# Optimization experiments

Hardware: AMD Instinct MI355X
Metric: run time of the kernel (lower is better)

## Reference

```python
import jax, jax.numpy as jnp
import numpy as np

THRE = 0.0
VOXEL = (160.0, 160.0)
MAX_N = 100  # module caps N at 100


def setup_inputs() -> dict:
    key = jax.random.key(0)
    k1, k2, k3 = jax.random.split(key, 3)
    # boxes in meters, scaled so BEV coords (x + W/2)/voxel fall inside [-1,1]
    pred_box_infra = jax.random.normal(k1, (100, 8, 3), dtype=jnp.float32) * 20.0
    pred_score_infra = jax.random.uniform(k2, (100,), dtype=jnp.float32)
    infra_features = jax.random.normal(k3, (1, 256, 256, 256), dtype=jnp.float32)
    return {
        "pred_box_infra": pred_box_infra,
        "pred_score_infra": pred_score_infra,
        "infra_features": infra_features,
    }


def _grid_sample_points(feat, grid):
    """torch.F.grid_sample (bilinear, zero padding, align_corners=False)
    specialized to a point list. feat: [C,H,W], grid: [N,2] with (x,y) in [-1,1].
    Returns [C,N]."""
    C, H, W = feat.shape
    ix = ((grid[:, 0] + 1.0) * W - 1.0) / 2.0
    iy = ((grid[:, 1] + 1.0) * H - 1.0) / 2.0
    x0 = jnp.floor(ix)
    y0 = jnp.floor(iy)
    x1 = x0 + 1.0
    y1 = y0 + 1.0
    wx1 = ix - x0
    wx0 = 1.0 - wx1
    wy1 = iy - y0
    wy0 = 1.0 - wy1

    def gather(xf, yf):
        xi = xf.astype(jnp.int32)
        yi = yf.astype(jnp.int32)
        valid = (xi >= 0) & (xi < W) & (yi >= 0) & (yi < H)
        xi = jnp.clip(xi, 0, W - 1)
        yi = jnp.clip(yi, 0, H - 1)
        v = feat[:, yi, xi]  # [C,N]
        return v * valid.astype(feat.dtype)

    return (gather(x0, y0) * (wx0 * wy0)
            + gather(x1, y0) * (wx1 * wy0)
            + gather(x0, y1) * (wx0 * wy1)
            + gather(x1, y1) * (wx1 * wy1))


def reference(pred_box_infra, pred_score_infra, infra_features):
    B, C, H, W = infra_features.shape
    # threshold filter; size=MAX_N keeps shapes static (all boxes pass by construction)
    idx = jnp.nonzero(pred_score_infra > THRE, size=MAX_N, fill_value=0)[0]
    boxes = pred_box_infra[idx]              # [N,8,3]
    N = MAX_N

    l = boxes.min(axis=1)                    # [N,3]
    r = boxes.max(axis=1)                    # [N,3]
    center = (l + r) / 2.0

    lx = (l[:, 0] + W / 2.0) / VOXEL[0]
    ly = (l[:, 1] + H / 2.0) / VOXEL[1]
    rx = (r[:, 0] + W / 2.0) / VOXEL[0]
    ry = (r[:, 1] + H / 2.0) / VOXEL[1]
    bev_size = (ry - ly) * (rx - lx)         # [N]

    cx = (center[:, 0] + W / 2.0) / VOXEL[0]
    cy = (center[:, 1] + H / 2.0) / VOXEL[1]
    grid = jnp.stack([cx, cy], axis=1)       # [N,2]

    cpf = _grid_sample_points(infra_features[0], grid)  # [C,N]

    X = jnp.arange(W, dtype=jnp.float32)
    Y = jnp.arange(H, dtype=jnp.float32)
    # gaussian exponent maps (no exp in original): [N,H,W]
    g = ((X[None, None, :] - cx[:, None, None]) ** 2
         + (Y[None, :, None] - cy[:, None, None]) ** 2) / (2.0 * bev_size[:, None, None] ** 2)

    out = jnp.einsum('cn,nhw->chw', cpf, g) / N  # [C,H,W]
    return out[None]                              # [1,C,H,W]
```

## Files before the change

### kernel.cpp

```cpp
#include <hip/hip_runtime.h>

namespace {

constexpr int CH    = 256;
constexpr int HH    = 256;
constexpr int WW    = 256;
constexpr int NBOX  = 100;
constexpr int MAXN  = 100;
constexpr int BLOCK = 512;
constexpr int SPLIT = 2;

__global__ __launch_bounds__(BLOCK) void comm_kernel(
    const float* __restrict__ boxes,
    const float* __restrict__ scores,
    const float* __restrict__ feat,
    float* __restrict__ out)
{
    __shared__ float sh_a[NBOX], sh_cx[NBOX], sh_cy[NBOX];
    __shared__ float sh_w00[NBOX], sh_w10[NBOX], sh_w01[NBOX], sh_w11[NBOX];
    __shared__ int   sh_t00[NBOX], sh_t10[NBOX], sh_t01[NBOX], sh_t11[NBOX];
    __shared__ int   sh_idx[MAXN];
    __shared__ int   sh_w0cnt;
    __shared__ float red[BLOCK / 64][4];
    __shared__ float sS[4];

    const int tid  = threadIdx.x;
    const int c    = blockIdx.x / SPLIT;
    const int half = blockIdx.x % SPLIT;

    bool p = false;
    if (tid < NBOX) p = scores[tid] > 0.0f;
    unsigned long long mask = __ballot(p);
    if (tid == 0) sh_w0cnt = (int)__popcll(mask);
    if (tid < MAXN) sh_idx[tid] = 0;

    if (tid < NBOX) {
        const float* bp = boxes + tid * 24;
        float lx = bp[0], ly = bp[1];
        float rx = lx,    ry = ly;
        #pragma unroll
        for (int k = 1; k < 8; ++k) {
            float x = bp[k * 3 + 0], y = bp[k * 3 + 1];
            lx = fminf(lx, x); rx = fmaxf(rx, x);
            ly = fminf(ly, y); ry = fmaxf(ry, y);
        }
        const float inv_vox = 1.0f / 160.0f;
        float cx = ((lx + rx) * 0.5f + 128.0f) * inv_vox;
        float cy = ((ly + ry) * 0.5f + 128.0f) * inv_vox;
        float lxn = (lx + 128.0f) * inv_vox, rxn = (rx + 128.0f) * inv_vox;
        float lyn = (ly + 128.0f) * inv_vox, ryn = (ry + 128.0f) * inv_vox;
        float bev = (ryn - lyn) * (rxn - lxn);
        sh_a[tid]  = 1.0f / (2.0f * bev * bev);
        sh_cx[tid] = cx;
        sh_cy[tid] = cy;

        float ix = ((cx + 1.0f) * (float)WW - 1.0f) * 0.5f;
        float iy = ((cy + 1.0f) * (float)HH - 1.0f) * 0.5f;
        float x0f = floorf(ix), y0f = floorf(iy);
        float wx1 = ix - x0f, wx0 = 1.0f - wx1;
        float wy1 = iy - y0f, wy0 = 1.0f - wy1;
        int x0 = (int)x0f, y0 = (int)y0f;
        int x1 = x0 + 1,  y1 = y0 + 1;
        bool vx0 = (x0 >= 0) && (x0 < WW), vx1 = (x1 >= 0) && (x1 < WW);
        bool vy0 = (y0 >= 0) && (y0 < HH), vy1 = (y1 >= 0) && (y1 < HH);
        sh_w00[tid] = (vx0 && vy0) ? wx0 * wy0 : 0.0f;
        sh_w10[tid] = (vx1 && vy0) ? wx1 * wy0 : 0.0f;
        sh_w01[tid] = (vx0 && vy1) ? wx0 * wy1 : 0.0f;
        sh_w11[tid] = (vx1 && vy1) ? wx1 * wy1 : 0.0f;
        int cx0 = min(max(x0, 0), WW - 1), cx1 = min(max(x1, 0), WW - 1);
        int cy0 = min(max(y0, 0), HH - 1), cy1 = min(max(y1, 0), HH - 1);
        sh_t00[tid] = cy0 * WW + cx0;
        sh_t10[tid] = cy0 * WW + cx1;
        sh_t01[tid] = cy1 * WW + cx0;
        sh_t11[tid] = cy1 * WW + cx1;
    }
    __syncthreads();

    if (p) {
        int lane = tid & 63;
        int pos  = (tid >= 64 ? sh_w0cnt : 0)
                 + (int)__popcll(mask & ((1ull << lane) - 1ull));
        sh_idx[pos] = tid;
    }
    __syncthreads();

    float S0 = 0.0f, S1 = 0.0f, S2 = 0.0f, S3 = 0.0f;
    if (tid < MAXN) {
        const int j = sh_idx[tid];
        const float* fc = feat + (size_t)c * (HH * WW);
        float cpf = fc[sh_t00[j]] * sh_w00[j]
                  + fc[sh_t10[j]] * sh_w10[j]
                  + fc[sh_t01[j]] * sh_w01[j]
                  + fc[sh_t11[j]] * sh_w11[j];
        float pa = cpf * sh_a[j];
        float cx = sh_cx[j], cy = sh_cy[j];
        S0 = pa;
        S1 = pa * cx;
        S2 = pa * cy;
        S3 = pa * (cx * cx + cy * cy);
    }
    #pragma unroll
    for (int off = 32; off > 0; off >>= 1) {
        S0 += __shfl_down(S0, off);
        S1 += __shfl_down(S1, off);
        S2 += __shfl_down(S2, off);
        S3 += __shfl_down(S3, off);
    }
    if ((tid & 63) == 0) {
        int wv = tid >> 6;
        red[wv][0] = S0; red[wv][1] = S1; red[wv][2] = S2; red[wv][3] = S3;
    }
    __syncthreads();
    if (tid == 0) {
        float t0 = 0, t1 = 0, t2 = 0, t3 = 0;
        #pragma unroll
        for (int wv = 0; wv < BLOCK / 64; ++wv) {
            t0 += red[wv][0]; t1 += red[wv][1];
            t2 += red[wv][2]; t3 += red[wv][3];
        }
        const float invN = 1.0f / (float)MAXN;
        sS[0] = t0 * invN; sS[1] = t1 * invN;
        sS[2] = t2 * invN; sS[3] = t3 * invN;
    }
    __syncthreads();

    const float s0 = sS[0], s1 = sS[1], s2 = sS[2], s3 = sS[3];
    float4* oc = (float4*)(out + (size_t)c * (HH * WW));
    const int nvec = (HH * WW) / 4;
    const int per  = nvec / SPLIT;
    const int beg  = half * per;

    const float wbase = (float)(((beg + tid) & 63) << 2);
    float4 wq;
    {
        float w0 = wbase, w1 = wbase + 1.0f, w2 = wbase + 2.0f, w3 = wbase + 3.0f;
        wq.x = s0 * (w0 * w0) - 2.0f * w0 * s1;
        wq.y = s0 * (w1 * w1) - 2.0f * w1 * s1;
        wq.z = s0 * (w2 * w2) - 2.0f * w2 * s1;
        wq.w = s0 * (w3 * w3) - 2.0f * w3 * s1;
    }
    for (int i = beg + tid; i < beg + per; i += BLOCK) {
        float hf = (float)(i >> 6);
        float hterm = s0 * (hf * hf) - 2.0f * hf * s2 + s3;
        float4 v;
        v.x = wq.x + hterm;
        v.y = wq.y + hterm;
        v.z = wq.z + hterm;
        v.w = wq.w + hterm;
        oc[i] = v;
    }
}

}

extern "C" void kernel_launch(void* const* d_in, const int* in_sizes, int n_in,
                              void* d_out, int out_size, void* d_ws, size_t ws_size,
                              hipStream_t stream) {
    const float* boxes  = (const float*)d_in[0];
    const float* scores = (const float*)d_in[1];
    const float* feat   = (const float*)d_in[2];
    float* out = (float*)d_out;
    comm_kernel<<<dim3(CH * SPLIT), dim3(BLOCK), 0, stream>>>(boxes, scores, feat, out);
}
```

Before: 18.81 us.

## Split into setup and fill kernels with more fill blocks and nontemporal stores

Separates the per-channel moment computation (box reduction plus bilinear gather) into a small setup kernel that writes four scalars per channel to workspace. A second fill kernel launches 8 blocks of 256 threads per channel to write the quadratic-form output with fully unrolled loops and nontemporal stores. This removes redundant per-block setup work and raises parallelism for the 64 MB store-bound phase, at the cost of an extra kernel launch and a workspace round trip.

New measurement: 20.92 us. +11.2%, slower.

```diff
diff --git a/kernel.cpp b/kernel.cpp
--- a/kernel.cpp
+++ b/kernel.cpp
@@ -7,26 +7,24 @@
 constexpr int WW    = 256;
 constexpr int NBOX  = 100;
 constexpr int MAXN  = 100;
-constexpr int BLOCK = 512;
-constexpr int SPLIT = 2;
 
-__global__ __launch_bounds__(BLOCK) void comm_kernel(
+typedef float f4 __attribute__((ext_vector_type(4)));
+
+__global__ __launch_bounds__(128) void setup_kernel(
     const float* __restrict__ boxes,
     const float* __restrict__ scores,
     const float* __restrict__ feat,
-    float* __restrict__ out)
+    float* __restrict__ S)
 {
     __shared__ float sh_a[NBOX], sh_cx[NBOX], sh_cy[NBOX];
     __shared__ float sh_w00[NBOX], sh_w10[NBOX], sh_w01[NBOX], sh_w11[NBOX];
     __shared__ int   sh_t00[NBOX], sh_t10[NBOX], sh_t01[NBOX], sh_t11[NBOX];
     __shared__ int   sh_idx[MAXN];
     __shared__ int   sh_w0cnt;
-    __shared__ float red[BLOCK / 64][4];
-    __shared__ float sS[4];
+    __shared__ float red[4];
 
-    const int tid  = threadIdx.x;
-    const int c    = blockIdx.x / SPLIT;
-    const int half = blockIdx.x % SPLIT;
+    const int tid = threadIdx.x;
+    const int c   = blockIdx.x;
 
     bool p = false;
     if (tid < NBOX) p = scores[tid] > 0.0f;
@@ -106,32 +104,37 @@
         S2 += __shfl_down(S2, off);
         S3 += __shfl_down(S3, off);
     }
-    if ((tid & 63) == 0) {
-        int wv = tid >> 6;
-        red[wv][0] = S0; red[wv][1] = S1; red[wv][2] = S2; red[wv][3] = S3;
-    }
+    if (tid == 64) { red[0] = S0; red[1] = S1; red[2] = S2; red[3] = S3; }
     __syncthreads();
     if (tid == 0) {
-        float t0 = 0, t1 = 0, t2 = 0, t3 = 0;
-        #pragma unroll
-        for (int wv = 0; wv < BLOCK / 64; ++wv) {
-            t0 += red[wv][0]; t1 += red[wv][1];
-            t2 += red[wv][2]; t3 += red[wv][3];
-        }
         const float invN = 1.0f / (float)MAXN;
-        sS[0] = t0 * invN; sS[1] = t1 * invN;
-        sS[2] = t2 * invN; sS[3] = t3 * invN;
+        f4 v;
+        v.x = (S0 + red[0]) * invN;
+        v.y = (S1 + red[1]) * invN;
+        v.z = (S2 + red[2]) * invN;
+        v.w = (S3 + red[3]) * invN;
+        *(f4*)(S + c * 4) = v;
     }
-    __syncthreads();
+}
 
-    const float s0 = sS[0], s1 = sS[1], s2 = sS[2], s3 = sS[3];
-    float4* oc = (float4*)(out + (size_t)c * (HH * WW));
-    const int nvec = (HH * WW) / 4;
-    const int per  = nvec / SPLIT;
-    const int beg  = half * per;
+constexpr int BLK_B   = 256;
+constexpr int BPC     = 8;
+constexpr int V_PER_C = (HH * WW) / 4;
+constexpr int V_PER_B = V_PER_C / BPC;
 
-    const float wbase = (float)(((beg + tid) & 63) << 2);
-    float4 wq;
+__global__ __launch_bounds__(BLK_B) void fill_kernel(
+    const float* __restrict__ S,
+    float* __restrict__ out)
+{
+    const int bid = blockIdx.x;
+    const int c   = bid >> 3;
+    const int tid = threadIdx.x;
+
+    const f4 s = *(const f4*)(S + c * 4);
+    const float s0 = s.x, s1 = s.y, s2 = s.z, s3 = s.w;
+
+    const float wbase = (float)((tid & 63) << 2);
+    f4 wq;
     {
         float w0 = wbase, w1 = wbase + 1.0f, w2 = wbase + 2.0f, w3 = wbase + 3.0f;
         wq.x = s0 * (w0 * w0) - 2.0f * w0 * s1;
@@ -139,15 +142,20 @@
         wq.z = s0 * (w2 * w2) - 2.0f * w2 * s1;
         wq.w = s0 * (w3 * w3) - 2.0f * w3 * s1;
     }
-    for (int i = beg + tid; i < beg + per; i += BLOCK) {
+
+    f4* oc = (f4*)(out + (size_t)c * (HH * WW));
+    const int beg = (bid & 7) * V_PER_B;
+    #pragma unroll
+    for (int it = 0; it < V_PER_B / BLK_B; ++it) {
+        int i = beg + it * BLK_B + tid;
         float hf = (float)(i >> 6);
         float hterm = s0 * (hf * hf) - 2.0f * hf * s2 + s3;
-        float4 v;
+        f4 v;
         v.x = wq.x + hterm;
         v.y = wq.y + hterm;
         v.z = wq.z + hterm;
         v.w = wq.w + hterm;
-        oc[i] = v;
+        __builtin_nontemporal_store(v, &oc[i]);
     }
 }
 
@@ -160,5 +168,8 @@
     const float* scores = (const float*)d_in[1];
     const float* feat   = (const float*)d_in[2];
     float* out = (float*)d_out;
-    comm_kernel<<<dim3(CH * SPLIT), dim3(BLOCK), 0, stream>>>(boxes, scores, feat, out);
+    float* S   = (float*)d_ws;
+
+    setup_kernel<<<dim3(CH), dim3(128), 0, stream>>>(boxes, scores, feat, S);
+    fill_kernel<<<dim3(CH * BPC), dim3(BLK_B), 0, stream>>>(S, out);
 }
```

## Drop shared-memory compaction, use nontemporal stores and smaller blocks with more splits

Applied to the files above, without the earlier changes.

Removes the shared-memory staging and index compaction of box data: each thread now computes its own box's bilinear sample and moment terms in registers, with the padded slots handled as (MAXN-cnt) copies of box 0's contribution via __syncthreads_count. Block size drops to 256 and each channel is split across 4 blocks, and the output loop is fully unrolled with nontemporal vector stores. The goal is fewer barriers and less prologue latency, plus streaming writes that bypass the cache. Correctness of the padding trick relies on thread 0's values standing for index 0.

Result: no change. 18.52 us (-1.5%).

```diff
diff --git a/kernel.cpp b/kernel.cpp
--- a/kernel.cpp
+++ b/kernel.cpp
@@ -7,8 +7,13 @@
 constexpr int WW    = 256;
 constexpr int NBOX  = 100;
 constexpr int MAXN  = 100;
-constexpr int BLOCK = 512;
-constexpr int SPLIT = 2;
+constexpr int BLOCK = 256;
+constexpr int SPLIT = 4;
+constexpr int VPC   = HH * WW / 4;
+constexpr int VPB   = VPC / SPLIT;
+constexpr int ITER  = VPB / BLOCK;
+
+typedef float f4 __attribute__((ext_vector_type(4)));
 
 __global__ __launch_bounds__(BLOCK) void comm_kernel(
     const float* __restrict__ boxes,
@@ -16,25 +21,20 @@
     const float* __restrict__ feat,
     float* __restrict__ out)
 {
-    __shared__ float sh_a[NBOX], sh_cx[NBOX], sh_cy[NBOX];
-    __shared__ float sh_w00[NBOX], sh_w10[NBOX], sh_w01[NBOX], sh_w11[NBOX];
-    __shared__ int   sh_t00[NBOX], sh_t10[NBOX], sh_t01[NBOX], sh_t11[NBOX];
-    __shared__ int   sh_idx[MAXN];
-    __shared__ int   sh_w0cnt;
     __shared__ float red[BLOCK / 64][4];
     __shared__ float sS[4];
 
     const int tid  = threadIdx.x;
-    const int c    = blockIdx.x / SPLIT;
-    const int half = blockIdx.x % SPLIT;
+    const int c    = blockIdx.x >> 2;
+    const int part = blockIdx.x & 3;
 
-    bool p = false;
-    if (tid < NBOX) p = scores[tid] > 0.0f;
-    unsigned long long mask = __ballot(p);
-    if (tid == 0) sh_w0cnt = (int)__popcll(mask);
-    if (tid < MAXN) sh_idx[tid] = 0;
+    int   pc = 0;
+    float T0 = 0.f, T1 = 0.f, T2 = 0.f, T3 = 0.f;
+    float U0 = 0.f, U1 = 0.f, U2 = 0.f, U3 = 0.f;
+    if (tid < NBOX) {
+        bool p = scores[tid] > 0.0f;
+        pc = p ? 1 : 0;
 
-    if (tid < NBOX) {
         const float* bp = boxes + tid * 24;
         float lx = bp[0], ly = bp[1];
         float rx = lx,    ry = ly;
@@ -50,9 +50,7 @@
         float lxn = (lx + 128.0f) * inv_vox, rxn = (rx + 128.0f) * inv_vox;
         float lyn = (ly + 128.0f) * inv_vox, ryn = (ry + 128.0f) * inv_vox;
         float bev = (ryn - lyn) * (rxn - lxn);
-        sh_a[tid]  = 1.0f / (2.0f * bev * bev);
-        sh_cx[tid] = cx;
-        sh_cy[tid] = cy;
+        float a   = 1.0f / (2.0f * bev * bev);
 
         float ix = ((cx + 1.0f) * (float)WW - 1.0f) * 0.5f;
         float iy = ((cy + 1.0f) * (float)HH - 1.0f) * 0.5f;
@@ -63,56 +61,43 @@
         int x1 = x0 + 1,  y1 = y0 + 1;
         bool vx0 = (x0 >= 0) && (x0 < WW), vx1 = (x1 >= 0) && (x1 < WW);
         bool vy0 = (y0 >= 0) && (y0 < HH), vy1 = (y1 >= 0) && (y1 < HH);
-        sh_w00[tid] = (vx0 && vy0) ? wx0 * wy0 : 0.0f;
-        sh_w10[tid] = (vx1 && vy0) ? wx1 * wy0 : 0.0f;
-        sh_w01[tid] = (vx0 && vy1) ? wx0 * wy1 : 0.0f;
-        sh_w11[tid] = (vx1 && vy1) ? wx1 * wy1 : 0.0f;
+        float w00 = (vx0 && vy0) ? wx0 * wy0 : 0.0f;
+        float w10 = (vx1 && vy0) ? wx1 * wy0 : 0.0f;
+        float w01 = (vx0 && vy1) ? wx0 * wy1 : 0.0f;
+        float w11 = (vx1 && vy1) ? wx1 * wy1 : 0.0f;
         int cx0 = min(max(x0, 0), WW - 1), cx1 = min(max(x1, 0), WW - 1);
         int cy0 = min(max(y0, 0), HH - 1), cy1 = min(max(y1, 0), HH - 1);
-        sh_t00[tid] = cy0 * WW + cx0;
-        sh_t10[tid] = cy0 * WW + cx1;
-        sh_t01[tid] = cy1 * WW + cx0;
-        sh_t11[tid] = cy1 * WW + cx1;
+
+        const float* fc = feat + (size_t)c * (HH * WW);
+        float cpf = fc[cy0 * WW + cx0] * w00
+                  + fc[cy0 * WW + cx1] * w10
+                  + fc[cy1 * WW + cx0] * w01
+                  + fc[cy1 * WW + cx1] * w11;
+
+        float pa = cpf * a;
+        U0 = pa;
+        U1 = pa * cx;
+        U2 = pa * cy;
+        U3 = pa * (cx * cx + cy * cy);
+        if (p) { T0 = U0; T1 = U1; T2 = U2; T3 = U3; }
     }
-    __syncthreads();
+    const int cnt = __syncthreads_count(pc);
 
-    if (p) {
-        int lane = tid & 63;
-        int pos  = (tid >= 64 ? sh_w0cnt : 0)
-                 + (int)__popcll(mask & ((1ull << lane) - 1ull));
-        sh_idx[pos] = tid;
-    }
-    __syncthreads();
-
-    float S0 = 0.0f, S1 = 0.0f, S2 = 0.0f, S3 = 0.0f;
-    if (tid < MAXN) {
-        const int j = sh_idx[tid];
-        const float* fc = feat + (size_t)c * (HH * WW);
-        float cpf = fc[sh_t00[j]] * sh_w00[j]
-                  + fc[sh_t10[j]] * sh_w10[j]
-                  + fc[sh_t01[j]] * sh_w01[j]
-                  + fc[sh_t11[j]] * sh_w11[j];
-        float pa = cpf * sh_a[j];
-        float cx = sh_cx[j], cy = sh_cy[j];
-        S0 = pa;
-        S1 = pa * cx;
-        S2 = pa * cy;
-        S3 = pa * (cx * cx + cy * cy);
-    }
     #pragma unroll
     for (int off = 32; off > 0; off >>= 1) {
-        S0 += __shfl_down(S0, off);
-        S1 += __shfl_down(S1, off);
-        S2 += __shfl_down(S2, off);
-        S3 += __shfl_down(S3, off);
+        T0 += __shfl_down(T0, off);
+        T1 += __shfl_down(T1, off);
+        T2 += __shfl_down(T2, off);
+        T3 += __shfl_down(T3, off);
     }
     if ((tid & 63) == 0) {
         int wv = tid >> 6;
-        red[wv][0] = S0; red[wv][1] = S1; red[wv][2] = S2; red[wv][3] = S3;
+        red[wv][0] = T0; red[wv][1] = T1; red[wv][2] = T2; red[wv][3] = T3;
     }
     __syncthreads();
     if (tid == 0) {
-        float t0 = 0, t1 = 0, t2 = 0, t3 = 0;
+        float e = (float)(MAXN - cnt);
+        float t0 = e * U0, t1 = e * U1, t2 = e * U2, t3 = e * U3;
         #pragma unroll
         for (int wv = 0; wv < BLOCK / 64; ++wv) {
             t0 += red[wv][0]; t1 += red[wv][1];
@@ -125,13 +110,9 @@
     __syncthreads();
 
     const float s0 = sS[0], s1 = sS[1], s2 = sS[2], s3 = sS[3];
-    float4* oc = (float4*)(out + (size_t)c * (HH * WW));
-    const int nvec = (HH * WW) / 4;
-    const int per  = nvec / SPLIT;
-    const int beg  = half * per;
 
-    const float wbase = (float)(((beg + tid) & 63) << 2);
-    float4 wq;
+    const float wbase = (float)((tid & 63) << 2);
+    f4 wq;
     {
         float w0 = wbase, w1 = wbase + 1.0f, w2 = wbase + 2.0f, w3 = wbase + 3.0f;
         wq.x = s0 * (w0 * w0) - 2.0f * w0 * s1;
@@ -139,15 +120,20 @@
         wq.z = s0 * (w2 * w2) - 2.0f * w2 * s1;
         wq.w = s0 * (w3 * w3) - 2.0f * w3 * s1;
     }
-    for (int i = beg + tid; i < beg + per; i += BLOCK) {
+
+    f4* oc = (f4*)(out + (size_t)c * (HH * WW));
+    const int beg = part * VPB;
+    #pragma unroll
+    for (int it = 0; it < ITER; ++it) {
+        int i = beg + it * BLOCK + tid;
         float hf = (float)(i >> 6);
         float hterm = s0 * (hf * hf) - 2.0f * hf * s2 + s3;
-        float4 v;
+        f4 v;
         v.x = wq.x + hterm;
         v.y = wq.y + hterm;
         v.z = wq.z + hterm;
         v.w = wq.w + hterm;
-        oc[i] = v;
+        __builtin_nontemporal_store(v, &oc[i]);
     }
 }
 
```
